# Performance work log

Measured on AMD Instinct MI355X. Metric: run time of the kernel, lower is better.

## Reference

```python
import jax, jax.numpy as jnp
import numpy as np

N, C, T, V = 16, 192, 120, 100
HEADS = 4
HEAD_CH = C // HEADS  # 48


def setup_inputs() -> dict:
    key = jax.random.key(0)
    ks = jax.random.split(key, 10)
    s = 0.05
    return {
        "x_q": jax.random.normal(ks[0], (N, C, T, V), jnp.float32),
        "x_kv": jax.random.normal(ks[1], (N, C, T, V), jnp.float32),
        "wq": jax.random.normal(ks[2], (C, C), jnp.float32) * s,
        "bq": jax.random.normal(ks[3], (C,), jnp.float32) * s,
        "wk": jax.random.normal(ks[4], (C, C), jnp.float32) * s,
        "bk": jax.random.normal(ks[5], (C,), jnp.float32) * s,
        "wp": jax.random.normal(ks[6], (C, C * HEADS), jnp.float32) * s,
        "bp": jax.random.normal(ks[7], (C,), jnp.float32) * s,
        "alphas": jnp.ones((1, HEADS, 1, 1), jnp.float32),
        "global_attn": jax.random.normal(ks[8], (1, 1, V, V), jnp.float32) * s,
    }


def reference(x_q, x_kv, wq, bq, wk, bk, wp, bp, alphas, global_attn):
    n, c, t, v = x_q.shape
    # 1x1 conv == pointwise linear over channel dim
    q = jnp.einsum('oc,nctv->notv', wq, x_q) + bq[None, :, None, None]
    k = jnp.einsum('oc,nctv->notv', wk, x_kv) + bk[None, :, None, None]
    q = q.reshape(n, HEADS, HEAD_CH, t, v)
    k = k.reshape(n, HEADS, HEAD_CH, t, v)
    # scores over (head_ch, T) contraction -> (N, heads, V, V)
    attn = jnp.tanh(jnp.einsum('nsctu,nsctv->nsuv', q, k) / (HEAD_CH * t))
    attn = attn * alphas + global_attn
    # aggregate full-channel x_kv per head: (N, heads, C, T, V)
    values = jnp.einsum('nctu,nsuv->nsctv', x_kv, attn)
    values = values.reshape(n, HEADS * c, t, v)
    out = jnp.einsum('oc,nctv->notv', wp, values) + bp[None, :, None, None]
    return out
```

## Files before the change

### kernel.cpp

```cpp
#include <hip/hip_runtime.h>

#define NN 16
#define CC 192
#define TT 120
#define VV 100
#define NH 4

typedef __attribute__((ext_vector_type(4))) float  float4v;
typedef __attribute__((ext_vector_type(8))) short  short8;
typedef __attribute__((ext_vector_type(2))) int    int2v;

#define MFMA16(A,B,Cacc) __builtin_amdgcn_mfma_f32_16x16x32_bf16(A,B,Cacc,0,0,0)

union S8U { unsigned u[4]; short8 s; };

__device__ __forceinline__ unsigned pk2(float a, float b) {
  union { float f; unsigned u; } x, y; x.f = a; y.f = b;
  return __builtin_amdgcn_perm(y.u, x.u, 0x07060302u);
}
__device__ __forceinline__ short b16t(float f) {
  union { float f; unsigned u; } x; x.f = f;
  return (short)(x.u >> 16);
}
__device__ __forceinline__ short f2b(float f) {
  union { float f; unsigned u; } x; x.f = f;
  unsigned r = x.u + 0x7fffu + ((x.u >> 16) & 1u);
  return (short)(r >> 16);
}

__global__ __launch_bounds__(256) void k_conv(const float* __restrict__ wq,
                                              const float* __restrict__ wk,
                                              const float* __restrict__ wp,
                                              short* __restrict__ wqF,
                                              short* __restrict__ wkF,
                                              short* __restrict__ wpF) {
  int i = blockIdx.x * 256 + threadIdx.x;
  if (i < CC*CC) {
    int o = i / CC, a = i % CC;
    int ct = o >> 4, l = o & 15, kc = a >> 5, q = (a & 31) >> 3, j = a & 7;
    int dst = ((ct*6 + kc)*64 + q*16 + l)*8 + j;
    wqF[dst] = f2b(wq[i]);
    wkF[dst] = f2b(wk[i]);
  }
  if (i < CC*CC*NH) {
    int o = i / (CC*NH), c2 = i % (CC*NH);
    int s = c2 / CC, cc = c2 % CC;
    int T = o >> 4, l = o & 15, kc = cc >> 5, q = (cc & 31) >> 3, j = cc & 7;
    int dst = (((s*12 + T)*6 + kc)*64 + q*16 + l)*8 + j;
    wpF[dst] = f2b(wp[i]);
  }
}

__global__ __launch_bounds__(448, 4) void k_qkS(const float* __restrict__ xq,
                                                const float* __restrict__ xkv,
                                                const short* __restrict__ wqF,
                                                const short* __restrict__ wkF,
                                                const float* __restrict__ bq,
                                                const float* __restrict__ bk,
                                                short* __restrict__ Qf,
                                                short* __restrict__ Kf) {
  __shared__ short XT[112*200];
  const int n = blockIdx.x / TT, t = blockIdx.x % TT;
  const int tid = threadIdx.x, w = tid >> 6, lane = tid & 63;
  const int q = lane >> 4, l15 = lane & 15;
  const size_t ns0 = (size_t)n*NH;

  #pragma unroll 1
  for (int ph = 0; ph < 2; ++ph) {
    const float* xb   = (ph ? xkv : xq) + (size_t)n*CC*TT*VV + t*VV;
    const short* wF   = ph ? wkF : wqF;
    const float* bias = ph ? bk : bq;
    short*       Of   = ph ? Kf : Qf;

    if (ph) __syncthreads();
    #pragma unroll 1
    for (int idx = tid; idx < 192*56; idx += 448) {
      int c = idx / 56, p = idx - c*56;
      int u = 2*p;
      int us = (u <= 98) ? u : 98;
      float2 f = *(const float2*)&xb[(size_t)c*(TT*VV) + us];
      XT[u*200 + c]       = b16t(f.x);
      XT[(u+1)*200 + c]   = b16t(f.y);
    }
    __syncthreads();

    short8 xf[6];
    #pragma unroll
    for (int kc = 0; kc < 6; ++kc)
      xf[kc] = *(const short8*)&XT[(16*w + l15)*200 + 32*kc + 8*q];

    #pragma unroll
    for (int ct = 0; ct < 12; ++ct) {
      float4v d = (float4v){0.f,0.f,0.f,0.f};
      #pragma unroll
      for (int kc = 0; kc < 6; ++kc) {
        short8 wf = *(const short8*)&wF[((ct*6 + kc)*64 + lane)*8];
        d = MFMA16(wf, xf[kc], d);
      }
      const float4v bv = *(const float4v*)&bias[16*ct + 4*q];
      const int sH = ct/3;
      const int kb = 48*t + 16*(ct - 3*sH);
      const int kq = kb + 4*q;
      const int kk = kq >> 5, q2 = (kq >> 3) & 3, j2 = kq & 7;
      size_t base = ((((ns0 + sH)*7 + w)*180 + kk)*64 + (q2*16 + l15))*8 + j2;
      int2v pr;
      pr.x = (int)pk2(d[0] + bv[0], d[1] + bv[1]);
      pr.y = (int)pk2(d[2] + bv[2], d[3] + bv[3]);
      *(int2v*)&Of[base] = pr;
    }
  }
}

__global__ __launch_bounds__(448, 4) void k_scores3(const short* __restrict__ Qf,
                                                    const short* __restrict__ Kf,
                                                    float* __restrict__ part2) {
  const int b = blockIdx.x;
  const int vh = b & 1, kc = (b >> 1) % 6, ns = b / 12;
  const int tid = threadIdx.x, w = tid >> 6, lane = tid & 63;
  const int q = lane >> 4, l15 = lane & 15;
  const short* Qb = Qf + (((size_t)ns*7 + w)*180 + kc*30)*512 + lane*8;
  const short* Kb = Kf + ((size_t)ns*7*180 + kc*30)*512 + lane*8;
  const int vt0 = vh ? 4 : 0, nvt = vh ? 3 : 4;

  float4v acc[4];
  #pragma unroll
  for (int j = 0; j < 4; ++j) acc[j] = (float4v){0.f,0.f,0.f,0.f};

  #pragma unroll 2
  for (int kk = 0; kk < 30; ++kk) {
    short8 aQ = *(const short8*)&Qb[(size_t)kk*512];
    #pragma unroll
    for (int j = 0; j < 4; ++j) {
      if (j < nvt) {
        short8 bK = *(const short8*)&Kb[((size_t)(vt0 + j)*180 + kk)*512];
        acc[j] = MFMA16(aQ, bK, acc[j]);
      }
    }
  }
  #pragma unroll
  for (int j = 0; j < 4; ++j) {
    if (j < nvt) {
      size_t p2 = (((size_t)ns*6 + kc)*112 + 16*(vt0 + j) + l15)*112 + 16*w + 4*q;
      __builtin_nontemporal_store(acc[j], (float4v*)&part2[p2]);
    }
  }
}

__global__ __launch_bounds__(256) void k_reduce2(const float* __restrict__ part2,
                                                 const float* __restrict__ alphas,
                                                 const float* __restrict__ ga,
                                                 short* __restrict__ attnT) {
  int bid = blockIdx.x;
  int ns = bid / 56, vc = bid % 56;
  int v = vc*2 + (threadIdx.x >> 7), u = threadIdx.x & 127;
  int s = ns & 3;
  float val = 0.f;
  if (v < VV && u < VV) {
    float sum = 0.f;
    #pragma unroll
    for (int kc = 0; kc < 6; ++kc)
      sum += __builtin_nontemporal_load(&part2[(((size_t)ns*6 + kc)*112 + v)*112 + u]);
    val = tanhf(sum * (1.f/5760.f)) * alphas[s] + ga[u*VV + v];
  }
  attnT[((size_t)ns*112 + v)*128 + u] = f2b(val);
}

__global__ __launch_bounds__(256, 2) void k_outE(const float* __restrict__ xkv,
                                                 const short* __restrict__ wpF,
                                                 const short* __restrict__ attnT,
                                                 const float* __restrict__ bp,
                                                 float* __restrict__ out) {
  __shared__ short YT[112*192];
  const int n = blockIdx.x / TT, t = blockIdx.x % TT;
  const int tid = threadIdx.x, w = tid >> 6, lane = tid & 63;
  const int q = lane >> 4, l15 = lane & 15;
  const unsigned swz = (unsigned)(l15 & 7) << 4;

  float4v accO[3][7];
  #pragma unroll
  for (int i = 0; i < 3; ++i)
    #pragma unroll
    for (int vt = 0; vt < 7; ++vt) accO[i][vt] = (float4v){0.f,0.f,0.f,0.f};

  short8   xh[3][3];
  unsigned xt3[3][2];
  #pragma unroll
  for (int i = 0; i < 3; ++i) {
    const float* xb = xkv + ((size_t)(n*CC + 16*(w + 4*i) + l15)*TT + t)*VV;
    #pragma unroll
    for (int ku = 0; ku < 3; ++ku) {
      const float4v A = *(const float4v*)(xb + 32*ku + 8*q);
      const float4v B = *(const float4v*)(xb + 32*ku + 8*q + 4);
      S8U sv; sv.u[0]=pk2(A[0],A[1]); sv.u[1]=pk2(A[2],A[3]);
      sv.u[2]=pk2(B[0],B[1]); sv.u[3]=pk2(B[2],B[3]);
      xh[i][ku] = sv.s;
    }
    if (q == 0) {
      const float4v A = *(const float4v*)(xb + 96);
      xt3[i][0] = pk2(A[0],A[1]); xt3[i][1] = pk2(A[2],A[3]);
    } else { xt3[i][0] = 0u; xt3[i][1] = 0u; }
  }

  #pragma unroll 1
  for (int s = 0; s < NH; ++s) {
    const short* aT = attnT + (size_t)((n*NH + s)*112)*128;

    __syncthreads();
    #pragma unroll
    for (int vt = 0; vt < 7; ++vt) {
      float4v y0 = (float4v){0.f,0.f,0.f,0.f};
      float4v y1 = y0, y2 = y0;
      #pragma unroll
      for (int ku = 0; ku < 4; ++ku) {
        short8 bv = *(const short8*)&aT[(16*vt + l15)*128 + 32*ku + 8*q];
        short8 a0, a1, a2;
        if (ku < 3) { a0 = xh[0][ku]; a1 = xh[1][ku]; a2 = xh[2][ku]; }
        else {
          S8U s0, s1, s2;
          s0.u[0]=xt3[0][0]; s0.u[1]=xt3[0][1]; s0.u[2]=0u; s0.u[3]=0u;
          s1.u[0]=xt3[1][0]; s1.u[1]=xt3[1][1]; s1.u[2]=0u; s1.u[3]=0u;
          s2.u[0]=xt3[2][0]; s2.u[1]=xt3[2][1]; s2.u[2]=0u; s2.u[3]=0u;
          a0 = s0.s; a1 = s1.s; a2 = s2.s;
        }
        y0 = MFMA16(a0, bv, y0);
        y1 = MFMA16(a1, bv, y1);
        y2 = MFMA16(a2, bv, y2);
      }
      int2v p0; p0.x = (int)pk2(y0[0], y0[1]); p0.y = (int)pk2(y0[2], y0[3]);
      int2v p1; p1.x = (int)pk2(y1[0], y1[1]); p1.y = (int)pk2(y1[2], y1[3]);
      int2v p2; p2.x = (int)pk2(y2[0], y2[1]); p2.y = (int)pk2(y2[2], y2[3]);
      unsigned bw = ((unsigned)(((16*vt + l15)*192 + 16*w + 4*q)*2)) ^ swz;
      *(int2v*)((char*)YT + bw)       = p0;
      *(int2v*)((char*)YT + bw + 128) = p1;
      *(int2v*)((char*)YT + bw + 256) = p2;
    }
    __syncthreads();

    #pragma unroll
    for (int kc2 = 0; kc2 < 6; ++kc2) {
      short8 ya[7];
      #pragma unroll
      for (int vt = 0; vt < 7; ++vt) {
        unsigned br = ((unsigned)(((16*vt + l15)*192 + 32*kc2 + 8*q)*2)) ^ swz;
        ya[vt] = *(const short8*)((char*)YT + br);
      }
      #pragma unroll
      for (int i = 0; i < 3; ++i) {
        short8 wf = *(const short8*)&wpF[(((s*12 + (w + 4*i))*6 + kc2)*64 + q*16 + l15)*8];
        #pragma unroll
        for (int vt = 0; vt < 7; ++vt)
          accO[i][vt] = MFMA16(ya[vt], wf, accO[i][vt]);
      }
    }
  }

  #pragma unroll
  for (int i = 0; i < 3; ++i) {
    int o = 16*(w + 4*i) + l15;
    float b = bp[o];
    #pragma unroll
    for (int vt = 0; vt < 7; ++vt) {
      int v0 = 16*vt + 4*q;
      if (v0 < VV) {
        float4v r = accO[i][vt];
        r[0] += b; r[1] += b; r[2] += b; r[3] += b;
        *(float4v*)&out[((size_t)(n*CC + o)*TT + t)*VV + v0] = r;
      }
    }
  }
}

extern "C" void kernel_launch(void* const* d_in, const int* in_sizes, int n_in,
                              void* d_out, int out_size, void* d_ws, size_t ws_size,
                              hipStream_t stream) {
  const float* xq     = (const float*)d_in[0];
  const float* xkv    = (const float*)d_in[1];
  const float* wq     = (const float*)d_in[2];
  const float* bq     = (const float*)d_in[3];
  const float* wk     = (const float*)d_in[4];
  const float* bk     = (const float*)d_in[5];
  const float* wp     = (const float*)d_in[6];
  const float* bp     = (const float*)d_in[7];
  const float* alphas = (const float*)d_in[8];
  const float* ga     = (const float*)d_in[9];
  float* out = (float*)d_out;
  char*  ws  = (char*)d_ws;

  short* wqF   = (short*)(ws);
  short* wkF   = (short*)(ws + 73728);
  short* wpF   = (short*)(ws + 147456);
  short* attnT = (short*)(ws + 442368);
  short* Qf    = (short*)(ws + 2277376);
  short* Kf    = (short*)(ws + 84852736ULL);
  float* part2 = (float*)(ws + 167428096ULL);

  hipLaunchKernelGGL(k_conv,    dim3(576),  dim3(256), 0, stream, wq, wk, wp, wqF, wkF, wpF);
  hipLaunchKernelGGL(k_qkS,     dim3(1920), dim3(448), 0, stream, xq, xkv, wqF, wkF, bq, bk, Qf, Kf);
  hipLaunchKernelGGL(k_scores3, dim3(768),  dim3(448), 0, stream, Qf, Kf, part2);
  hipLaunchKernelGGL(k_reduce2, dim3(3584), dim3(256), 0, stream, part2, alphas, ga, attnT);
  hipLaunchKernelGGL(k_outE,    dim3(1920), dim3(256), 0, stream, xkv, wpF, attnT, bp, out);
}
```

Before: 814.2 us.

## Fuse score reduction into scores kernel and shrink output-kernel LDS footprint

After: 1.029 ms. 26.4% more time.

```diff
diff --git a/kernel.cpp b/kernel.cpp
--- a/kernel.cpp
+++ b/kernel.cpp
@@ -33,7 +33,8 @@
                                               const float* __restrict__ wp,
                                               short* __restrict__ wqF,
                                               short* __restrict__ wkF,
-                                              short* __restrict__ wpF) {
+                                              short* __restrict__ wpF,
+                                              short* __restrict__ attnT) {
   int i = blockIdx.x * 256 + threadIdx.x;
   if (i < CC*CC) {
     int o = i / CC, a = i % CC;
@@ -48,6 +49,11 @@
     int T = o >> 4, l = o & 15, kc = cc >> 5, q = (cc & 31) >> 3, j = cc & 7;
     int dst = (((s*12 + T)*6 + kc)*64 + q*16 + l)*8 + j;
     wpF[dst] = f2b(wp[i]);
+  }
+  if (i < 64*112*16) {
+    int ns = i / (112*16), rem = i % (112*16);
+    int v = rem >> 4, uu = 112 + (rem & 15);
+    attnT[((size_t)ns*112 + v)*128 + uu] = 0;
   }
 }
 
@@ -111,66 +117,65 @@
   }
 }
 
-__global__ __launch_bounds__(448, 4) void k_scores3(const short* __restrict__ Qf,
+__global__ __launch_bounds__(256, 6) void k_scores4(const short* __restrict__ Qf,
                                                     const short* __restrict__ Kf,
-                                                    float* __restrict__ part2) {
-  const int b = blockIdx.x;
-  const int vh = b & 1, kc = (b >> 1) % 6, ns = b / 12;
+                                                    const float* __restrict__ alphas,
+                                                    const float* __restrict__ ga,
+                                                    short* __restrict__ attnT) {
+  __shared__ float SP[4][4][16][16];
+  const int b0 = blockIdx.x;
+  const int b  = (b0 & 7)*112 + (b0 >> 3);
+  const int vh = b & 1, ut = (b >> 1) % 7, ns = b / 14;
+  const int s = ns & 3;
   const int tid = threadIdx.x, w = tid >> 6, lane = tid & 63;
   const int q = lane >> 4, l15 = lane & 15;
-  const short* Qb = Qf + (((size_t)ns*7 + w)*180 + kc*30)*512 + lane*8;
-  const short* Kb = Kf + ((size_t)ns*7*180 + kc*30)*512 + lane*8;
   const int vt0 = vh ? 4 : 0, nvt = vh ? 3 : 4;
 
+  const short* Qb  = Qf + (((size_t)ns*7 + ut)*180 + w*45)*512 + lane*8;
+  const short* Kb0 = Kf + ((size_t)ns*7*180 + w*45)*512 + lane*8;
+
   float4v acc[4];
   #pragma unroll
   for (int j = 0; j < 4; ++j) acc[j] = (float4v){0.f,0.f,0.f,0.f};
 
-  #pragma unroll 2
-  for (int kk = 0; kk < 30; ++kk) {
+  #pragma unroll 3
+  for (int kk = 0; kk < 45; ++kk) {
     short8 aQ = *(const short8*)&Qb[(size_t)kk*512];
     #pragma unroll
     for (int j = 0; j < 4; ++j) {
       if (j < nvt) {
-        short8 bK = *(const short8*)&Kb[((size_t)(vt0 + j)*180 + kk)*512];
+        short8 bK = *(const short8*)&Kb0[((size_t)(vt0 + j)*180 + kk)*512];
         acc[j] = MFMA16(aQ, bK, acc[j]);
       }
     }
   }
   #pragma unroll
-  for (int j = 0; j < 4; ++j) {
+  for (int j = 0; j < 4; ++j)
     if (j < nvt) {
-      size_t p2 = (((size_t)ns*6 + kc)*112 + 16*(vt0 + j) + l15)*112 + 16*w + 4*q;
-      __builtin_nontemporal_store(acc[j], (float4v*)&part2[p2]);
-    }
-  }
-}
-
-__global__ __launch_bounds__(256) void k_reduce2(const float* __restrict__ part2,
-                                                 const float* __restrict__ alphas,
-                                                 const float* __restrict__ ga,
-                                                 short* __restrict__ attnT) {
-  int bid = blockIdx.x;
-  int ns = bid / 56, vc = bid % 56;
-  int v = vc*2 + (threadIdx.x >> 7), u = threadIdx.x & 127;
-  int s = ns & 3;
-  float val = 0.f;
-  if (v < VV && u < VV) {
-    float sum = 0.f;
-    #pragma unroll
-    for (int kc = 0; kc < 6; ++kc)
-      sum += __builtin_nontemporal_load(&part2[(((size_t)ns*6 + kc)*112 + v)*112 + u]);
-    val = tanhf(sum * (1.f/5760.f)) * alphas[s] + ga[u*VV + v];
-  }
-  attnT[((size_t)ns*112 + v)*128 + u] = f2b(val);
-}
-
-__global__ __launch_bounds__(256, 2) void k_outE(const float* __restrict__ xkv,
+      #pragma unroll
+      for (int r = 0; r < 4; ++r)
+        SP[w][j][4*q + r][l15] = acc[j][r];
+    }
+  __syncthreads();
+
+  const int ncell = nvt << 8;
+  for (int cell = tid; cell < ncell; cell += 256) {
+    int j = cell >> 8, rc = cell & 255, vr = rc >> 4, uc = rc & 15;
+    float sum = SP[0][j][uc][vr] + SP[1][j][uc][vr] + SP[2][j][uc][vr] + SP[3][j][uc][vr];
+    int u = ut*16 + uc, v = 16*(vt0 + j) + vr;
+    float val = 0.f;
+    if (u < VV && v < VV)
+      val = tanhf(sum * (1.f/5760.f)) * alphas[s] + ga[u*VV + v];
+    attnT[((size_t)ns*112 + v)*128 + u] = f2b(val);
+  }
+}
+
+__global__ __launch_bounds__(256, 3) void k_outF(const float* __restrict__ xkv,
                                                  const short* __restrict__ wpF,
                                                  const short* __restrict__ attnT,
                                                  const float* __restrict__ bp,
                                                  float* __restrict__ out) {
-  __shared__ short YT[112*192];
+  __shared__ short YT[VV*192];
   const int n = blockIdx.x / TT, t = blockIdx.x % TT;
   const int tid = threadIdx.x, w = tid >> 6, lane = tid & 63;
   const int q = lane >> 4, l15 = lane & 15;
@@ -226,13 +231,15 @@
         y1 = MFMA16(a1, bv, y1);
         y2 = MFMA16(a2, bv, y2);
       }
-      int2v p0; p0.x = (int)pk2(y0[0], y0[1]); p0.y = (int)pk2(y0[2], y0[3]);
-      int2v p1; p1.x = (int)pk2(y1[0], y1[1]); p1.y = (int)pk2(y1[2], y1[3]);
-      int2v p2; p2.x = (int)pk2(y2[0], y2[1]); p2.y = (int)pk2(y2[2], y2[3]);
-      unsigned bw = ((unsigned)(((16*vt + l15)*192 + 16*w + 4*q)*2)) ^ swz;
-      *(int2v*)((char*)YT + bw)       = p0;
-      *(int2v*)((char*)YT + bw + 128) = p1;
-      *(int2v*)((char*)YT + bw + 256) = p2;
+      if (16*vt + l15 < VV) {
+        int2v p0; p0.x = (int)pk2(y0[0], y0[1]); p0.y = (int)pk2(y0[2], y0[3]);
+        int2v p1; p1.x = (int)pk2(y1[0], y1[1]); p1.y = (int)pk2(y1[2], y1[3]);
+        int2v p2; p2.x = (int)pk2(y2[0], y2[1]); p2.y = (int)pk2(y2[2], y2[3]);
+        unsigned bw = ((unsigned)(((16*vt + l15)*192 + 16*w + 4*q)*2)) ^ swz;
+        *(int2v*)((char*)YT + bw)       = p0;
+        *(int2v*)((char*)YT + bw + 128) = p1;
+        *(int2v*)((char*)YT + bw + 256) = p2;
+      }
     }
     __syncthreads();
 
@@ -241,7 +248,9 @@
       short8 ya[7];
       #pragma unroll
       for (int vt = 0; vt < 7; ++vt) {
-        unsigned br = ((unsigned)(((16*vt + l15)*192 + 32*kc2 + 8*q)*2)) ^ swz;
+        int row = 16*vt + l15;
+        row = (row < VV) ? row : (VV-1);
+        unsigned br = ((unsigned)((row*192 + 32*kc2 + 8*q)*2)) ^ swz;
         ya[vt] = *(const short8*)((char*)YT + br);
       }
       #pragma unroll
@@ -292,11 +301,9 @@
   short* attnT = (short*)(ws + 442368);
   short* Qf    = (short*)(ws + 2277376);
   short* Kf    = (short*)(ws + 84852736ULL);
-  float* part2 = (float*)(ws + 167428096ULL);
-
-  hipLaunchKernelGGL(k_conv,    dim3(576),  dim3(256), 0, stream, wq, wk, wp, wqF, wkF, wpF);
+
+  hipLaunchKernelGGL(k_conv,    dim3(576),  dim3(256), 0, stream, wq, wk, wp, wqF, wkF, wpF, attnT);
   hipLaunchKernelGGL(k_qkS,     dim3(1920), dim3(448), 0, stream, xq, xkv, wqF, wkF, bq, bk, Qf, Kf);
-  hipLaunchKernelGGL(k_scores3, dim3(768),  dim3(448), 0, stream, Qf, Kf, part2);
-  hipLaunchKernelGGL(k_reduce2, dim3(3584), dim3(256), 0, stream, part2, alphas, ga, attnT);
-  hipLaunchKernelGGL(k_outE,    dim3(1920), dim3(256), 0, stream, xkv, wpF, attnT, bp, out);
-}
+  hipLaunchKernelGGL(k_scores4, dim3(896),  dim3(256), 0, stream, Qf, Kf, alphas, ga, attnT);
+  hipLaunchKernelGGL(k_outF,    dim3(1920), dim3(256), 0, stream, xkv, wpF, attnT, bp, out);
+}
```
